# Optimization experiments

Hardware: AMD Instinct MI355X
Metric: run time of the kernel (lower is better)

The kernel has to match this reference:

```python
import jax, jax.numpy as jnp
import numpy as np

NUM_HEADS = 32
NUM_KV_HEADS = 8
HEAD_DIM = 128
SLIDING_WINDOW = 1024
ROPE_THETA = 10000.0


def _rotate_half(x):
    x1, x2 = jnp.split(x, 2, axis=-1)
    return jnp.concatenate((-x2, x1), axis=-1)


def _rope_cos_sin(seq_len, head_dim, theta, dtype):
    inv_freq = 1.0 / (theta ** (jnp.arange(0, head_dim, 2, dtype=jnp.float32) / head_dim))
    t = jnp.arange(seq_len, dtype=jnp.float32)
    freqs = t[:, None] * inv_freq[None, :]            # [S, hd/2]
    emb = jnp.concatenate((freqs, freqs), axis=-1)     # [S, hd]
    return jnp.cos(emb).astype(dtype), jnp.sin(emb).astype(dtype)


def setup_inputs() -> dict:
    key = jax.random.key(0)
    ks = jax.random.split(key, 5)
    B, S, H = 2, 2048, 4096
    kv_dim = NUM_KV_HEADS * HEAD_DIM
    scale = 1.0 / np.sqrt(H)
    return {
        "hidden_states": jax.random.normal(ks[0], (B, S, H), dtype=jnp.float32),
        "Wq": jax.random.normal(ks[1], (H, H), dtype=jnp.float32) * scale,
        "Wk": jax.random.normal(ks[2], (H, kv_dim), dtype=jnp.float32) * scale,
        "Wv": jax.random.normal(ks[3], (H, kv_dim), dtype=jnp.float32) * scale,
        "Wo": jax.random.normal(ks[4], (H, H), dtype=jnp.float32) * scale,
    }


def reference(hidden_states, Wq, Wk, Wv, Wo):
    B, S, H = hidden_states.shape
    groups = NUM_HEADS // NUM_KV_HEADS

    q = (hidden_states @ Wq).reshape(B, S, NUM_HEADS, HEAD_DIM).transpose(0, 2, 1, 3)
    k = (hidden_states @ Wk).reshape(B, S, NUM_KV_HEADS, HEAD_DIM).transpose(0, 2, 1, 3)
    v = (hidden_states @ Wv).reshape(B, S, NUM_KV_HEADS, HEAD_DIM).transpose(0, 2, 1, 3)

    cos, sin = _rope_cos_sin(S, HEAD_DIM, ROPE_THETA, q.dtype)  # [S, hd]
    q = q * cos + _rotate_half(q) * sin
    k = k * cos + _rotate_half(k) * sin

    # GQA: repeat_interleave kv heads to match query heads
    k = jnp.repeat(k, groups, axis=1)
    v = jnp.repeat(v, groups, axis=1)

    scores = jnp.einsum("bhqd,bhkd->bhqk", q, k) / np.sqrt(HEAD_DIM)

    i = jnp.arange(S)[:, None]
    j = jnp.arange(S)[None, :]
    allowed = (j <= i) & (i - j <= SLIDING_WINDOW // 2)  # causal + sliding window
    scores = jnp.where(allowed[None, None], scores, jnp.float32(-1e30))

    probs = jax.nn.softmax(scores, axis=-1)
    out = jnp.einsum("bhqk,bhkd->bhqd", probs, v)        # [B, nH, S, hd]
    out = out.transpose(0, 2, 1, 3).reshape(B, S, NUM_HEADS * HEAD_DIM)
    return out @ Wo
```

## Files before the change

kernel.cpp:

```cpp
#include <hip/hip_runtime.h>
#include <hip/hip_bf16.h>
#include <math.h>

#define BB 2
#define SS 2048
#define HH 4096
#define NH 32
#define NKV 8
#define HD 128
#define KVD (NKV*HD)
#define WIN 512
#define MROWS (BB*SS)

#define DT_BF16 1
#define DT_F32  2

typedef __hip_bfloat16 bf16;
typedef __attribute__((ext_vector_type(8))) short short8;
typedef __attribute__((ext_vector_type(4))) float f32x4;

__device__ __forceinline__ float ldf(const bf16* p){ return __bfloat162float(*p); }
__device__ __forceinline__ float ldf(const float* p){ return *p; }
__device__ __forceinline__ void stf(bf16* p, float v){ *p = __float2bfloat16(v); }
__device__ __forceinline__ void stf(float* p, float v){ *p = v; }

__global__ void detect_kernel(const void* __restrict__ w, int* __restrict__ flag)
{
  __shared__ int big;
  if (threadIdx.x == 0) big = 0;
  __syncthreads();
  const unsigned short* u = (const unsigned short*)w;
  for (int i = threadIdx.x; i < 2048; i += 256) {
    int ex = (u[i] >> 7) & 0xFF;
    if (ex >= 160) big = 1;
  }
  __syncthreads();
  if (threadIdx.x == 0) *flag = big ? DT_F32 : DT_BF16;
}

__global__ __launch_bounds__(256)
void cvt_x(const int* __restrict__ flag, const float* __restrict__ X,
           bf16* __restrict__ Y)
{
  if (*flag != DT_F32) return;
  const size_t idx = (size_t)blockIdx.x*256 + threadIdx.x;
  const f32x4 a = *(const f32x4*)(X + idx*8);
  const f32x4 b = *(const f32x4*)(X + idx*8 + 4);
  union { short8 s; bf16 h[8]; } u;
  #pragma unroll
  for (int j = 0; j < 4; j++) {
    u.h[j]     = __float2bfloat16(a[j]);
    u.h[j + 4] = __float2bfloat16(b[j]);
  }
  *(short8*)(Y + idx*8) = u.s;
}

template<typename TS>
__global__ __launch_bounds__(256)
void transpose_cvt(const int* __restrict__ flag, int mydt,
                   const TS* __restrict__ W, bf16* __restrict__ WT, int Kd, int Nd)
{
  if (*flag != mydt) return;
  __shared__ float tile[32][33];
  const int n0 = blockIdx.x*32, k0 = blockIdx.y*32;
  const int tx = threadIdx.x & 31, ty = threadIdx.x >> 5;
  #pragma unroll
  for (int j = 0; j < 4; j++)
    tile[ty + j*8][tx] = ldf(W + (size_t)(k0 + ty + j*8)*Nd + n0 + tx);
  __syncthreads();
  #pragma unroll
  for (int j = 0; j < 4; j++)
    WT[(size_t)(n0 + ty + j*8)*Kd + k0 + tx] = __float2bfloat16(tile[tx][ty + j*8]);
}

#define MFMA16(a,b,c) __builtin_amdgcn_mfma_f32_16x16x32_bf16(a,b,c,0,0,0)

template<typename TC>
__global__ __launch_bounds__(512)
void gemm256(const int* __restrict__ flag, int mydt,
             const bf16* __restrict__ A, const bf16* __restrict__ Bm,
             TC* __restrict__ C, int M, int N, int K)
{
  if (*flag != mydt) return;
  __shared__ __align__(16) bf16 lds[65536];
  const int tid = threadIdx.x;
  const int w = tid >> 6, lane = tid & 63;
  const int wm = w >> 2, wn = w & 3;
  const int fr = lane & 15, fq = lane >> 4;

  const int gx = gridDim.x;
  int wg = blockIdx.y*gx + blockIdx.x;
  const int cpx = (gx*gridDim.y) >> 3;
  wg = (wg & 7)*cpx + (wg >> 3);
  const int tM = (wg / gx)*256, tN = (wg % gx)*256;

  const int NT = K >> 6;

  auto stage = [&](int tt, int s){
    const int dbuf = tt & 1;
    const int hf = s & 1;
    const bf16* src = (s < 2) ? A : Bm;
    const int brow = ((s < 2) ? tM : tN) + hf*128;
    const int cbase = ((s < 2) ? 0 : 4096) + (dbuf*2 + hf)*1024;
    #pragma unroll
    for (int g = 0; g < 2; g++) {
      const int Ch = g*512 + tid;
      const int r = Ch >> 3, c = Ch & 7;
      const int cs = c ^ (r & 7);
      const bf16* gp = src + (size_t)(brow + r)*K + tt*64 + cs*8;
      char* lp = (char*)lds + (size_t)(cbase + g*512 + w*64)*16;
      __builtin_amdgcn_global_load_lds((const __attribute__((address_space(1))) void*)gp,
                                       (__attribute__((address_space(3))) void*)lp, 16, 0, 0);
    }
  };
  auto rdA = [&](int dbuf, int m, int kk) -> short8 {
    const int r = m*16 + fr;
    const int chunk = (dbuf*2 + wm)*1024 + r*8 + ((kk*4 + fq) ^ (r & 7));
    return *(const short8*)((char*)lds + (size_t)chunk*16);
  };
  auto rdB = [&](int dbuf, int n, int kk) -> short8 {
    const int rg = wn*64 + n*16 + fr;
    const int hf = rg >> 7, rr = rg & 127;
    const int chunk = 4096 + (dbuf*2 + hf)*1024 + rr*8 + ((kk*4 + fq) ^ (rr & 7));
    return *(const short8*)((char*)lds + (size_t)chunk*16);
  };

  f32x4 acc[8][4] = {};

  #pragma unroll
  for (int s = 0; s < 4; s++) stage(0, s);
  stage(1, 0); stage(1, 1);
  asm volatile("s_waitcnt vmcnt(4)" ::: "memory");
  __builtin_amdgcn_s_barrier();

  short8 a0[4][2], a1[4][2], b0[2][2], b1[2][2];
  for (int kt = 0; kt < NT; kt++) {
    const int db = kt & 1;
    #pragma unroll
    for (int m = 0; m < 4; m++){ a0[m][0]=rdA(db,m,0); a0[m][1]=rdA(db,m,1); }
    #pragma unroll
    for (int n = 0; n < 2; n++){ b0[n][0]=rdB(db,n,0); b0[n][1]=rdB(db,n,1); }
    if (kt+1 < NT) stage(kt+1, 2);
    asm volatile("s_waitcnt lgkmcnt(0)" ::: "memory");
    __builtin_amdgcn_sched_barrier(0);
    __builtin_amdgcn_s_setprio(1);
    #pragma unroll
    for (int m = 0; m < 4; m++)
      #pragma unroll
      for (int n = 0; n < 2; n++){
        acc[m][n] = MFMA16(a0[m][0], b0[n][0], acc[m][n]);
        acc[m][n] = MFMA16(a0[m][1], b0[n][1], acc[m][n]);
      }
    __builtin_amdgcn_s_setprio(0);
    __builtin_amdgcn_s_barrier();
    #pragma unroll
    for (int m = 0; m < 4; m++){ a1[m][0]=rdA(db,m+4,0); a1[m][1]=rdA(db,m+4,1); }
    #pragma unroll
    for (int n = 0; n < 2; n++){ b1[n][0]=rdB(db,n+2,0); b1[n][1]=rdB(db,n+2,1); }
    if (kt+1 < NT) stage(kt+1, 3);
    asm volatile("s_waitcnt lgkmcnt(0)" ::: "memory");
    __builtin_amdgcn_sched_barrier(0);
    __builtin_amdgcn_s_setprio(1);
    #pragma unroll
    for (int m = 0; m < 4; m++)
      #pragma unroll
      for (int n = 0; n < 2; n++){
        acc[m+4][n+2] = MFMA16(a1[m][0], b1[n][0], acc[m+4][n+2]);
        acc[m+4][n+2] = MFMA16(a1[m][1], b1[n][1], acc[m+4][n+2]);
      }
    __builtin_amdgcn_s_setprio(0);
    __builtin_amdgcn_s_barrier();
    if (kt+2 < NT) stage(kt+2, 0);
    __builtin_amdgcn_s_setprio(1);
    #pragma unroll
    for (int m = 0; m < 4; m++)
      #pragma unroll
      for (int n = 0; n < 2; n++){
        acc[m][n+2] = MFMA16(a0[m][0], b1[n][0], acc[m][n+2]);
        acc[m][n+2] = MFMA16(a0[m][1], b1[n][1], acc[m][n+2]);
      }
    __builtin_amdgcn_s_setprio(0);
    __builtin_amdgcn_s_barrier();
    if (kt+2 < NT) stage(kt+2, 1);
    __builtin_amdgcn_s_setprio(1);
    #pragma unroll
    for (int m = 0; m < 4; m++)
      #pragma unroll
      for (int n = 0; n < 2; n++){
        acc[m+4][n] = MFMA16(a1[m][0], b0[n][0], acc[m+4][n]);
        acc[m+4][n] = MFMA16(a1[m][1], b0[n][1], acc[m+4][n]);
      }
    __builtin_amdgcn_s_setprio(0);
    if (kt+2 < NT) { asm volatile("s_waitcnt vmcnt(4)" ::: "memory"); }
    else           { asm volatile("s_waitcnt vmcnt(0)" ::: "memory"); }
    __builtin_amdgcn_s_barrier();
  }

  #pragma unroll
  for (int m = 0; m < 8; m++)
    #pragma unroll
    for (int n = 0; n < 4; n++)
      #pragma unroll
      for (int r = 0; r < 4; r++)
        stf(C + (size_t)(tM + wm*128 + m*16 + fq*4 + r)*N + (tN + wn*64 + n*16 + fr),
            acc[m][n][r]);
}

template<typename TC, int VTRANS>
__global__ __launch_bounds__(256)
void gemm_bt(const int* __restrict__ flag, int mydt,
             const bf16* __restrict__ A, const bf16* __restrict__ Bm,
             TC* __restrict__ C, int M, int N, int K)
{
  if (*flag != mydt) return;
  __shared__ __align__(16) bf16 As[128*32];
  __shared__ __align__(16) bf16 Bs[128*32];
  const int tid  = threadIdx.x;
  const int w    = tid >> 6;
  const int lane = tid & 63;
  const int wr = w >> 1, wc = w & 1;
  const int tM = blockIdx.y*128, tN = blockIdx.x*128;
  const int srow = tid >> 2;
  const int scol = (tid & 3) * 8;
  const int fr = lane & 15;
  const int kq = (lane >> 4) * 8;

  f32x4 acc[4][4] = {};

  for (int k0 = 0; k0 < K; k0 += 32) {
    __syncthreads();
    #pragma unroll
    for (int q = 0; q < 2; q++) {
      const int row = q*64 + srow;
      const bf16* ga = A  + (size_t)(tM + row)*K + k0 + scol;
      const bf16* gb = Bm + (size_t)(tN + row)*K + k0 + scol;
      char* la = (char*)As + q*4096 + w*1024;
      char* lb = (char*)Bs + q*4096 + w*1024;
      __builtin_amdgcn_global_load_lds((const __attribute__((address_space(1))) void*)ga,
                                       (__attribute__((address_space(3))) void*)la, 16, 0, 0);
      __builtin_amdgcn_global_load_lds((const __attribute__((address_space(1))) void*)gb,
                                       (__attribute__((address_space(3))) void*)lb, 16, 0, 0);
    }
    __syncthreads();

    short8 af[4], bfr[4];
    #pragma unroll
    for (int m = 0; m < 4; m++) af[m]  = *(const short8*)&As[(wr*64 + m*16 + fr)*32 + kq];
    #pragma unroll
    for (int n = 0; n < 4; n++) bfr[n] = *(const short8*)&Bs[(wc*64 + n*16 + fr)*32 + kq];
    #pragma unroll
    for (int m = 0; m < 4; m++)
      #pragma unroll
      for (int n = 0; n < 4; n++)
        acc[m][n] = MFMA16(af[m], bfr[n], acc[m][n]);
  }

  const int fq = lane >> 4;
  #pragma unroll
  for (int m = 0; m < 4; m++)
    #pragma unroll
    for (int n = 0; n < 4; n++)
      #pragma unroll
      for (int r = 0; r < 4; r++) {
        const int gm = tM + wr*64 + m*16 + fq*4 + r;
        const int gn = tN + wc*64 + n*16 + fr;
        if constexpr (VTRANS) {
          size_t idx = ((size_t)((gm >> 11)*NKV + (gn >> 7)))*((size_t)HD*SS)
                     + (size_t)(gn & 127)*SS + (gm & 2047);
          stf((bf16*)C + idx, acc[m][n][r]);
        } else {
          stf(C + (size_t)gm*N + gn, acc[m][n][r]);
        }
      }
}

__global__ void rope_kernel(bf16* __restrict__ X, int nh)
{
  int idx = blockIdx.x*blockDim.x + threadIdx.x;
  int total = MROWS * nh * 64;
  if (idx >= total) return;
  int f   = idx & 63;
  int h   = (idx >> 6) % nh;
  int row = (idx >> 6) / nh;
  int s   = row & (SS - 1);
  float ang = (float)s * exp2f((float)f * -0.20762050593046014f);
  float sv, cv;
  __sincosf(ang, &sv, &cv);
  size_t base = (size_t)row*nh*HD + (size_t)h*HD;
  float x1 = ldf(X + base + f), x2 = ldf(X + base + 64 + f);
  stf(X + base + f,      x1*cv - x2*sv);
  stf(X + base + 64 + f, x2*cv + x1*sv);
}

__global__ __launch_bounds__(256, 2)
void attn_mfma(const bf16* __restrict__ Q, const bf16* __restrict__ K,
               const bf16* __restrict__ VT, bf16* __restrict__ Aout)
{
  const int i0 = blockIdx.x * 64;
  const int h  = blockIdx.y;
  const int b  = blockIdx.z;
  const int kh = h >> 2;
  const int tid = threadIdx.x;
  const int w = tid >> 6, lane = tid & 63;
  const int fr = lane & 15, fq = lane >> 4;

  __shared__ __align__(16) bf16 Qs[64*128];
  __shared__ __align__(16) bf16 Ks[64*128];
  __shared__ __align__(16) bf16 Vs[128*64];
  __shared__ __align__(16) bf16 Ps[4][16*64];

  {
    const bf16* gq = Q + (size_t)(b*SS + i0)*HH + h*HD;
    #pragma unroll
    for (int it = 0; it < 4; it++) {
      int slot = tid + it*256;
      int r = slot >> 4, cg = slot & 15;
      short8 v = *(const short8*)(gq + (size_t)r*HH + cg*8);
      *(short8*)((char*)Qs + r*256 + ((cg*16) ^ ((r & 7) << 4))) = v;
    }
  }
  __syncthreads();

  short8 qf[4];
  {
    const int qrow = w*16 + fr;
    #pragma unroll
    for (int kk = 0; kk < 4; kk++)
      qf[kk] = *(const short8*)((char*)Qs + qrow*256 + ((kk*64 + fq*16) ^ ((qrow & 7) << 4)));
  }

  const float scale = 0.08838834764831845f;
  f32x4 o[8];
  #pragma unroll
  for (int nn = 0; nn < 8; nn++) o[nn] = (f32x4){0.f, 0.f, 0.f, 0.f};
  float m_run[4] = {-1e30f, -1e30f, -1e30f, -1e30f};
  float l_run[4] = {0.f, 0.f, 0.f, 0.f};

  const int j0_lo = (i0 >= WIN) ? (i0 - WIN) : 0;

  for (int j0 = j0_lo; j0 <= i0; j0 += 64) {
    __syncthreads();
    {
      const bf16* gk = K + (size_t)(b*SS + j0)*KVD + kh*HD;
      #pragma unroll
      for (int it = 0; it < 4; it++) {
        int slot = tid + it*256;
        int r = slot >> 4, cg = slot & 15;
        short8 v = *(const short8*)(gk + (size_t)r*KVD + cg*8);
        *(short8*)((char*)Ks + r*256 + ((cg*16) ^ ((r & 7) << 4))) = v;
      }
    }
    {
      const bf16* gv = VT + ((size_t)(b*NKV + kh)*HD)*SS + j0;
      #pragma unroll
      for (int it = 0; it < 4; it++) {
        int slot = tid + it*256;
        int d = slot >> 3, jg = slot & 7;
        short8 v = *(const short8*)(gv + (size_t)d*SS + jg*8);
        *(short8*)((char*)Vs + d*128 + ((jg*16) ^ ((d & 7) << 4))) = v;
      }
    }
    __syncthreads();

    f32x4 sv[4];
    #pragma unroll
    for (int jf = 0; jf < 4; jf++) sv[jf] = (f32x4){0.f, 0.f, 0.f, 0.f};
    #pragma unroll
    for (int kk = 0; kk < 4; kk++) {
      #pragma unroll
      for (int jf = 0; jf < 4; jf++) {
        const int krow = jf*16 + fr;
        short8 kf = *(const short8*)((char*)Ks + krow*256 + ((kk*64 + fq*16) ^ ((krow & 7) << 4)));
        sv[jf] = MFMA16(qf[kk], kf, sv[jf]);
      }
    }

    const bool needmask = !((j0 >= i0 - 448) && (j0 <= i0 - 64));
    #pragma unroll
    for (int jf = 0; jf < 4; jf++)
      #pragma unroll
      for (int r = 0; r < 4; r++) {
        float x = sv[jf][r] * scale;
        if (needmask) {
          int iq = i0 + w*16 + fq*4 + r;
          int jv = j0 + jf*16 + fr;
          if (jv > iq || iq - jv > WIN) x = -1e30f;
        }
        sv[jf][r] = x;
      }

    float fac[4];
    #pragma unroll
    for (int r = 0; r < 4; r++) {
      float t = fmaxf(fmaxf(sv[0][r], sv[1][r]), fmaxf(sv[2][r], sv[3][r]));
      t = fmaxf(t, __shfl_xor(t, 1));
      t = fmaxf(t, __shfl_xor(t, 2));
      t = fmaxf(t, __shfl_xor(t, 4));
      t = fmaxf(t, __shfl_xor(t, 8));
      float mn = fmaxf(m_run[r], t);
      fac[r] = __expf(m_run[r] - mn);
      m_run[r] = mn;
    }
    #pragma unroll
    for (int r = 0; r < 4; r++) {
      float sum = 0.f;
      #pragma unroll
      for (int jf = 0; jf < 4; jf++) {
        float p = __expf(sv[jf][r] - m_run[r]);
        sv[jf][r] = p;
        sum += p;
      }
      sum += __shfl_xor(sum, 1);
      sum += __shfl_xor(sum, 2);
      sum += __shfl_xor(sum, 4);
      sum += __shfl_xor(sum, 8);
      l_run[r] = l_run[r]*fac[r] + sum;
    }

    char* pbase = (char*)(&Ps[w][0]);
    #pragma unroll
    for (int jf = 0; jf < 4; jf++)
      #pragma unroll
      for (int r = 0; r < 4; r++) {
        int q = fq*4 + r, j = jf*16 + fr;
        *(bf16*)(pbase + q*128 + ((j*2) ^ ((q & 7) << 4))) = __float2bfloat16(sv[jf][r]);
      }

    #pragma unroll
    for (int nn = 0; nn < 8; nn++)
      #pragma unroll
      for (int r = 0; r < 4; r++) o[nn][r] *= fac[r];

    #pragma unroll
    for (int kt = 0; kt < 2; kt++) {
      short8 ap = *(const short8*)(pbase + fr*128 + ((kt*64 + fq*16) ^ ((fr & 7) << 4)));
      #pragma unroll
      for (int nn = 0; nn < 8; nn++) {
        const int d = nn*16 + fr;
        short8 vf = *(const short8*)((char*)Vs + d*128 + ((kt*64 + fq*16) ^ ((d & 7) << 4)));
        o[nn] = MFMA16(ap, vf, o[nn]);
      }
    }
  }

  float inv[4];
  #pragma unroll
  for (int r = 0; r < 4; r++) inv[r] = 1.0f / l_run[r];
  bf16* ao = Aout + (size_t)(b*SS + i0 + w*16)*HH + h*HD;
  #pragma unroll
  for (int nn = 0; nn < 8; nn++)
    #pragma unroll
    for (int r = 0; r < 4; r++)
      stf(ao + (size_t)(fq*4 + r)*HH + nn*16 + fr, o[nn][r] * inv[r]);
}

extern "C" void kernel_launch(void* const* d_in, const int* in_sizes, int n_in,
                              void* d_out, int out_size, void* d_ws, size_t ws_size,
                              hipStream_t stream)
{
  char* ws = (char*)d_ws;
  const size_t MB = (size_t)1 << 20;
  int*  flag = (int*)ws;
  bf16* Q  = (bf16*)(ws + 256);
  bf16* K  = (bf16*)(ws + 256 + 32*MB);
  bf16* VT = (bf16*)(ws + 256 + 40*MB);
  bf16* S  = (bf16*)(ws + 256 + 48*MB);
  bf16* WTo = Q;
  bf16* Xb = (bf16*)d_out;

  detect_kernel<<<1, 256, 0, stream>>>(d_in[1], flag);
  cvt_x<<<MROWS*HH/8/256, 256, 0, stream>>>(flag, (const float*)d_in[0], Xb);

  auto tr = [&](const void* W, int Kd, int Nd, bf16* dst){
    dim3 g(Nd/32, Kd/32);
    transpose_cvt<bf16 ><<<g,256,0,stream>>>(flag, DT_BF16, (const bf16 *)W, dst, Kd, Nd);
    transpose_cvt<float><<<g,256,0,stream>>>(flag, DT_F32 , (const float*)W, dst, Kd, Nd);
  };

  tr(d_in[1], HH, HH, S);
  {
    dim3 g(HH/256, MROWS/256);
    gemm256<bf16><<<g,512,0,stream>>>(flag, DT_BF16, (const bf16*)d_in[0], S, Q, MROWS, HH, HH);
    gemm256<bf16><<<g,512,0,stream>>>(flag, DT_F32 , Xb,                   S, Q, MROWS, HH, HH);
  }
  tr(d_in[2], HH, KVD, S);
  {
    dim3 g(KVD/128, MROWS/128);
    gemm_bt<bf16,0><<<g,256,0,stream>>>(flag, DT_BF16, (const bf16*)d_in[0], S, K, MROWS, KVD, HH);
    gemm_bt<bf16,0><<<g,256,0,stream>>>(flag, DT_F32 , Xb,                   S, K, MROWS, KVD, HH);
  }
  tr(d_in[3], HH, KVD, S);
  {
    dim3 g(KVD/128, MROWS/128);
    gemm_bt<bf16,1><<<g,256,0,stream>>>(flag, DT_BF16, (const bf16*)d_in[0], S, VT, MROWS, KVD, HH);
    gemm_bt<bf16,1><<<g,256,0,stream>>>(flag, DT_F32 , Xb,                   S, VT, MROWS, KVD, HH);
  }

  rope_kernel<<<(MROWS*NH *64 + 255)/256, 256, 0, stream>>>(Q, NH);
  rope_kernel<<<(MROWS*NKV*64 + 255)/256, 256, 0, stream>>>(K, NKV);
  attn_mfma<<<dim3(SS/64, NH, BB), 256, 0, stream>>>(Q, K, VT, S);

  tr(d_in[4], HH, HH, WTo);
  {
    dim3 g(HH/256, MROWS/256);
    gemm256<bf16 ><<<g,512,0,stream>>>(flag, DT_BF16, S, WTo, (bf16 *)d_out, MROWS, HH, HH);
    gemm256<float><<<g,512,0,stream>>>(flag, DT_F32 , S, WTo, (float*)d_out, MROWS, HH, HH);
  }
}
```

Baseline: 788.0 us.

## Batch K and V projections into one launch and add barriers in gemm256

```diff
diff --git a/kernel.cpp b/kernel.cpp
--- a/kernel.cpp
+++ b/kernel.cpp
@@ -58,9 +58,12 @@
 template<typename TS>
 __global__ __launch_bounds__(256)
 void transpose_cvt(const int* __restrict__ flag, int mydt,
-                   const TS* __restrict__ W, bf16* __restrict__ WT, int Kd, int Nd)
+                   const TS* __restrict__ W0, const TS* __restrict__ W1,
+                   bf16* __restrict__ D0, bf16* __restrict__ D1, int Kd, int Nd)
 {
   if (*flag != mydt) return;
+  const TS* W  = blockIdx.z ? W1 : W0;
+  bf16*    WT  = blockIdx.z ? D1 : D0;
   __shared__ float tile[32][33];
   const int n0 = blockIdx.x*32, k0 = blockIdx.y*32;
   const int tx = threadIdx.x & 31, ty = threadIdx.x >> 5;
@@ -141,6 +144,8 @@
     #pragma unroll
     for (int n = 0; n < 2; n++){ b0[n][0]=rdB(db,n,0); b0[n][1]=rdB(db,n,1); }
     if (kt+1 < NT) stage(kt+1, 2);
+    asm volatile("s_waitcnt lgkmcnt(8)" ::: "memory");
+    __builtin_amdgcn_s_barrier();
     asm volatile("s_waitcnt lgkmcnt(0)" ::: "memory");
     __builtin_amdgcn_sched_barrier(0);
     __builtin_amdgcn_s_setprio(1);
@@ -158,6 +163,8 @@
     #pragma unroll
     for (int n = 0; n < 2; n++){ b1[n][0]=rdB(db,n+2,0); b1[n][1]=rdB(db,n+2,1); }
     if (kt+1 < NT) stage(kt+1, 3);
+    asm volatile("s_waitcnt lgkmcnt(8)" ::: "memory");
+    __builtin_amdgcn_s_barrier();
     asm volatile("s_waitcnt lgkmcnt(0)" ::: "memory");
     __builtin_amdgcn_sched_barrier(0);
     __builtin_amdgcn_s_setprio(1);
@@ -171,6 +178,7 @@
     __builtin_amdgcn_s_setprio(0);
     __builtin_amdgcn_s_barrier();
     if (kt+2 < NT) stage(kt+2, 0);
+    __builtin_amdgcn_s_barrier();
     __builtin_amdgcn_s_setprio(1);
     #pragma unroll
     for (int m = 0; m < 4; m++)
@@ -182,6 +190,7 @@
     __builtin_amdgcn_s_setprio(0);
     __builtin_amdgcn_s_barrier();
     if (kt+2 < NT) stage(kt+2, 1);
+    __builtin_amdgcn_s_barrier();
     __builtin_amdgcn_s_setprio(1);
     #pragma unroll
     for (int m = 0; m < 4; m++)
@@ -206,13 +215,14 @@
             acc[m][n][r]);
 }
 
-template<typename TC, int VTRANS>
 __global__ __launch_bounds__(256)
-void gemm_bt(const int* __restrict__ flag, int mydt,
-             const bf16* __restrict__ A, const bf16* __restrict__ Bm,
-             TC* __restrict__ C, int M, int N, int K)
+void gemm_kv(const int* __restrict__ flag, int mydt, const bf16* __restrict__ A,
+             const bf16* __restrict__ WTk, const bf16* __restrict__ WTv,
+             bf16* __restrict__ Kout, bf16* __restrict__ VTout, int M, int N, int K)
 {
   if (*flag != mydt) return;
+  const bool vpath = blockIdx.z != 0;
+  const bf16* Bm = vpath ? WTv : WTk;
   __shared__ __align__(16) bf16 As[128*32];
   __shared__ __align__(16) bf16 Bs[128*32];
   const int tid  = threadIdx.x;
@@ -264,12 +274,12 @@
       for (int r = 0; r < 4; r++) {
         const int gm = tM + wr*64 + m*16 + fq*4 + r;
         const int gn = tN + wc*64 + n*16 + fr;
-        if constexpr (VTRANS) {
+        if (vpath) {
           size_t idx = ((size_t)((gm >> 11)*NKV + (gn >> 7)))*((size_t)HD*SS)
                      + (size_t)(gn & 127)*SS + (gm & 2047);
-          stf((bf16*)C + idx, acc[m][n][r]);
+          stf(VTout + idx, acc[m][n][r]);
         } else {
-          stf(C + (size_t)gm*N + gn, acc[m][n][r]);
+          stf(Kout + (size_t)gm*N + gn, acc[m][n][r]);
         }
       }
 }
@@ -465,42 +475,40 @@
   bf16* K  = (bf16*)(ws + 256 + 32*MB);
   bf16* VT = (bf16*)(ws + 256 + 40*MB);
   bf16* S  = (bf16*)(ws + 256 + 48*MB);
+  bf16* WTk = S;
+  bf16* WTv = S + (size_t)KVD*HH;
   bf16* WTo = Q;
   bf16* Xb = (bf16*)d_out;
 
   detect_kernel<<<1, 256, 0, stream>>>(d_in[1], flag);
   cvt_x<<<MROWS*HH/8/256, 256, 0, stream>>>(flag, (const float*)d_in[0], Xb);
 
-  auto tr = [&](const void* W, int Kd, int Nd, bf16* dst){
-    dim3 g(Nd/32, Kd/32);
-    transpose_cvt<bf16 ><<<g,256,0,stream>>>(flag, DT_BF16, (const bf16 *)W, dst, Kd, Nd);
-    transpose_cvt<float><<<g,256,0,stream>>>(flag, DT_F32 , (const float*)W, dst, Kd, Nd);
+  auto tr1 = [&](const void* W, int Kd, int Nd, bf16* dst){
+    dim3 g(Nd/32, Kd/32, 1);
+    transpose_cvt<bf16 ><<<g,256,0,stream>>>(flag, DT_BF16, (const bf16 *)W, (const bf16 *)W, dst, dst, Kd, Nd);
+    transpose_cvt<float><<<g,256,0,stream>>>(flag, DT_F32 , (const float*)W, (const float*)W, dst, dst, Kd, Nd);
   };
 
-  tr(d_in[1], HH, HH, S);
+  tr1(d_in[1], HH, HH, S);
   {
     dim3 g(HH/256, MROWS/256);
     gemm256<bf16><<<g,512,0,stream>>>(flag, DT_BF16, (const bf16*)d_in[0], S, Q, MROWS, HH, HH);
     gemm256<bf16><<<g,512,0,stream>>>(flag, DT_F32 , Xb,                   S, Q, MROWS, HH, HH);
   }
-  tr(d_in[2], HH, KVD, S);
   {
-    dim3 g(KVD/128, MROWS/128);
-    gemm_bt<bf16,0><<<g,256,0,stream>>>(flag, DT_BF16, (const bf16*)d_in[0], S, K, MROWS, KVD, HH);
-    gemm_bt<bf16,0><<<g,256,0,stream>>>(flag, DT_F32 , Xb,                   S, K, MROWS, KVD, HH);
-  }
-  tr(d_in[3], HH, KVD, S);
-  {
-    dim3 g(KVD/128, MROWS/128);
-    gemm_bt<bf16,1><<<g,256,0,stream>>>(flag, DT_BF16, (const bf16*)d_in[0], S, VT, MROWS, KVD, HH);
-    gemm_bt<bf16,1><<<g,256,0,stream>>>(flag, DT_F32 , Xb,                   S, VT, MROWS, KVD, HH);
+    dim3 gt(KVD/32, HH/32, 2);
+    transpose_cvt<bf16 ><<<gt,256,0,stream>>>(flag, DT_BF16, (const bf16 *)d_in[2], (const bf16 *)d_in[3], WTk, WTv, HH, KVD);
+    transpose_cvt<float><<<gt,256,0,stream>>>(flag, DT_F32 , (const float*)d_in[2], (const float*)d_in[3], WTk, WTv, HH, KVD);
+    dim3 g(KVD/128, MROWS/128, 2);
+    gemm_kv<<<g,256,0,stream>>>(flag, DT_BF16, (const bf16*)d_in[0], WTk, WTv, K, VT, MROWS, KVD, HH);
+    gemm_kv<<<g,256,0,stream>>>(flag, DT_F32 , Xb,                   WTk, WTv, K, VT, MROWS, KVD, HH);
   }
 
   rope_kernel<<<(MROWS*NH *64 + 255)/256, 256, 0, stream>>>(Q, NH);
   rope_kernel<<<(MROWS*NKV*64 + 255)/256, 256, 0, stream>>>(K, NKV);
   attn_mfma<<<dim3(SS/64, NH, BB), 256, 0, stream>>>(Q, K, VT, S);
 
-  tr(d_in[4], HH, HH, WTo);
+  tr1(d_in[4], HH, HH, WTo);
   {
     dim3 g(HH/256, MROWS/256);
     gemm256<bf16 ><<<g,512,0,stream>>>(flag, DT_BF16, S, WTo, (bf16 *)d_out, MROWS, HH, HH);
```

Measured after the change: 734.5 us. -6.8%, faster.
